# Optimization experiments

Hardware: AMD Instinct MI355X
Metric: run time of the kernel (lower is better)

## Reference

```python
import jax, jax.numpy as jnp
import numpy as np

H = 16          # num_heads
HD = 64         # head_dim = latent_dim // num_heads
RHD = 32        # rope_head_dim = head_dim // 2
NHD = 32        # nope_head_dim
Q_LAT = 256     # latent_dim // compression_ratio
KV_LAT = 204    # xf_latent_dim // (compression_ratio + 1)
MAX_LEN = 2048
THETA = 10000.0
EPS = 1e-5


def _rope_tables():
    half = RHD // 2  # 16
    freqs = 1.0 / THETA ** (np.arange(half, dtype=np.float32) / half)
    t = np.arange(MAX_LEN, dtype=np.float32)
    ang = np.outer(t, freqs)  # (MAX_LEN, half)
    return jnp.asarray(np.cos(ang)), jnp.asarray(np.sin(ang))

COS, SIN = _rope_tables()


def _ln(x, g, b):
    m = jnp.mean(x, axis=-1, keepdims=True)
    v = jnp.var(x, axis=-1, keepdims=True)
    return (x - m) * jax.lax.rsqrt(v + EPS) * g + b


def _rope(t, cos, sin):
    # t: (..., L, RHD); cos/sin: (L, RHD//2); interleaved even/odd convention
    ev, od = t[..., 0::2], t[..., 1::2]
    oe = ev * cos - od * sin
    oo = ev * sin + od * cos
    return jnp.stack([oe, oo], axis=-1).reshape(t.shape)


def setup_inputs() -> dict:
    key = jax.random.key(0)
    ks = jax.random.split(key, 12)
    D = 1024
    s = 0.02
    return {
        "x": jax.random.normal(ks[0], (2, 2048, D), jnp.float32),
        "xf": jax.random.normal(ks[1], (2, 2048, D), jnp.float32),
        "Wqc": jax.random.normal(ks[2], (D, Q_LAT), jnp.float32) * s,
        "gq": jnp.ones((Q_LAT,), jnp.float32),
        "bq": jnp.zeros((Q_LAT,), jnp.float32),
        "Wq_rope": jax.random.normal(ks[3], (Q_LAT, H * RHD), jnp.float32) * s,
        "Wq_nope": jax.random.normal(ks[4], (Q_LAT, H * NHD), jnp.float32) * s,
        "Wkvc": jax.random.normal(ks[5], (D, KV_LAT), jnp.float32) * s,
        "gkv": jnp.ones((KV_LAT,), jnp.float32),
        "bkv": jnp.zeros((KV_LAT,), jnp.float32),
        "Wk_nope": jax.random.normal(ks[6], (KV_LAT, H * NHD), jnp.float32) * s,
        "Wv": jax.random.normal(ks[7], (KV_LAT, H * HD), jnp.float32) * s,
        "Wkr": jax.random.normal(ks[8], (D, RHD), jnp.float32) * s,
        "Wo": jax.random.normal(ks[9], (D, D), jnp.float32) * s,
        "bo": jnp.zeros((D,), jnp.float32),
    }


def reference(x, xf, Wqc, gq, bq, Wq_rope, Wq_nope, Wkvc, gkv, bkv, Wk_nope, Wv, Wkr, Wo, bo):
    B, T, D = x.shape
    S = xf.shape[1]

    # query path: compress -> LN -> decoupled decompress
    ql = _ln(x @ Wqc, gq, bq)                                   # (B,T,Q_LAT)
    q_nope = (ql @ Wq_nope).reshape(B, T, H, NHD).transpose(0, 2, 1, 3)  # (B,H,T,NHD)
    q_rope = (ql @ Wq_rope).reshape(B, T, H, RHD).transpose(0, 2, 1, 3)  # (B,H,T,RHD)

    # key/value path: compress -> LN -> decompress; shared single rope head
    kvl = _ln(xf @ Wkvc, gkv, bkv)                              # (B,S,KV_LAT)
    k_nope = (kvl @ Wk_nope).reshape(B, S, H, NHD).transpose(0, 2, 1, 3)  # (B,H,S,NHD)
    v = (kvl @ Wv).reshape(B, S, H, HD).transpose(0, 2, 1, 3)   # (B,H,S,HD)
    k_rope = (xf @ Wkr).reshape(B, S, 1, RHD).transpose(0, 2, 1, 3)       # (B,1,S,RHD)

    q_rope = _rope(q_rope, COS[:T], SIN[:T])
    k_rope = _rope(k_rope, COS[:S], SIN[:S]) / H
    k_rope = jnp.broadcast_to(k_rope, (B, H, S, RHD))

    q = jnp.concatenate([q_nope, q_rope], axis=-1)              # (B,H,T,HD)
    k = jnp.concatenate([k_nope, k_rope], axis=-1)              # (B,H,S,HD)

    scale = 1.0 / jnp.sqrt(jnp.asarray(HD, q.dtype))
    scores = jnp.einsum("bhtd,bhsd->bhts", q, k) * scale
    attn = jax.nn.softmax(scores, axis=-1)
    o = jnp.einsum("bhts,bhsd->bhtd", attn, v)                  # (B,H,T,HD)
    o = o.transpose(0, 2, 1, 3).reshape(B, T, H * HD)
    return o @ Wo + bo
```

## Files before the change

### kernel.cpp

```cpp
#include <hip/hip_runtime.h>
#include <hip/hip_bf16.h>
#include <math.h>

#define SEQ 2048

typedef __bf16 bf16x8 __attribute__((ext_vector_type(8)));
typedef float  f32x4  __attribute__((ext_vector_type(4)));

__device__ __forceinline__ unsigned short f2bf(float f) {
  __bf16 h = (__bf16)f;
  return __builtin_bit_cast(unsigned short, h);
}

__device__ __forceinline__ void gload16(const unsigned short* g, unsigned short* l) {
  __builtin_amdgcn_global_load_lds(
      (const __attribute__((address_space(1))) void*)g,
      (__attribute__((address_space(3))) void*)l, 16, 0, 0);
}

#define CLOG (0.125f * 1.44269504f)

struct WPrep {
  const float* src[8];
  unsigned short* dst[8];
  int K[8], N[8], NR[8], KC[8], nb[8];
  float2* cst;
};

__global__ __launch_bounds__(256) void wprep_kernel(WPrep p)
{
  __shared__ float tile[32][33];
  int bid = blockIdx.x;
  if (bid < 128) {
    const int idx = bid * 256 + threadIdx.x;
    const int pos = idx >> 4, i = idx & 15;
    const float freq = exp2f(-(float)i * 0.8304820237f);
    const float ang = (float)pos * freq;
    p.cst[idx] = make_float2(cosf(ang), sinf(ang));
    return;
  }
  bid -= 128;
  int di = 0;
  while (bid >= p.nb[di]) { bid -= p.nb[di]; ++di; }
  const float* src = p.src[di];
  unsigned short* dst = p.dst[di];
  const int K = p.K[di], N = p.N[di], KC = p.KC[di];
  const int nkx = KC >> 5;
  const int k0 = (bid % nkx) * 32, n0 = (bid / nkx) * 32;
  const int tx = threadIdx.x & 31, ty = threadIdx.x >> 5;
  for (int r = ty; r < 32; r += 8) {
    const int k = k0 + r, n = n0 + tx;
    tile[r][tx] = (k < K && n < N) ? src[(long)k * N + n] : 0.0f;
  }
  __syncthreads();
  for (int r = ty; r < 32; r += 8) {
    const int n = n0 + r, k = k0 + tx;
    dst[(long)n * KC + k] = f2bf(tile[tx][r]);
  }
}

template <int EPI, bool AF32>
__device__ __forceinline__ void gemm_body(
    unsigned short* smem,
    const void* __restrict__ Av, const unsigned short* __restrict__ BT,
    const float* __restrict__ bias, const float2* __restrict__ cst,
    void* __restrict__ C0v, void* __restrict__ C1v, int K, int N,
    int bx, int by)
{
  unsigned short* As = smem;
  unsigned short* Bs = smem + 2 * 128 * 32;
  const int tid = threadIdx.x;
  const int w = tid >> 6, lane = tid & 63;
  const int ln16 = lane & 15, quad = lane >> 4;
  const int wm = (w >> 1) * 64, wn = (w & 1) * 64;
  const int m0 = by * 128, n0 = bx * 128;
  const int rr = tid >> 2, cc = (tid & 3) * 8;

  const unsigned short* A = (const unsigned short*)Av;
  const float* Af = (const float*)Av;

  auto stageB = [&](int ib, int k0) {
    gload16(&BT[(long)(n0 + rr)      * K + k0 + cc], &Bs[ib * 4096 + rr * 32 + cc]);
    gload16(&BT[(long)(n0 + 64 + rr) * K + k0 + cc], &Bs[ib * 4096 + (64 + rr) * 32 + cc]);
  };
  auto stageAbf = [&](int ib, int k0) {
    gload16(&A[(long)(m0 + rr)      * K + k0 + cc], &As[ib * 4096 + rr * 32 + cc]);
    gload16(&A[(long)(m0 + 64 + rr) * K + k0 + cc], &As[ib * 4096 + (64 + rr) * 32 + cc]);
  };
  auto writeAf32 = [&](int ib, const float4& a0, const float4& a1,
                       const float4& a2, const float4& a3) {
    ushort4 u;
    u.x = f2bf(a0.x); u.y = f2bf(a0.y); u.z = f2bf(a0.z); u.w = f2bf(a0.w);
    *(ushort4*)&As[ib * 4096 + rr * 32 + cc] = u;
    u.x = f2bf(a1.x); u.y = f2bf(a1.y); u.z = f2bf(a1.z); u.w = f2bf(a1.w);
    *(ushort4*)&As[ib * 4096 + rr * 32 + cc + 4] = u;
    u.x = f2bf(a2.x); u.y = f2bf(a2.y); u.z = f2bf(a2.z); u.w = f2bf(a2.w);
    *(ushort4*)&As[ib * 4096 + (64 + rr) * 32 + cc] = u;
    u.x = f2bf(a3.x); u.y = f2bf(a3.y); u.z = f2bf(a3.z); u.w = f2bf(a3.w);
    *(ushort4*)&As[ib * 4096 + (64 + rr) * 32 + cc + 4] = u;
  };

  f32x4 acc[4][4];
#pragma unroll
  for (int i = 0; i < 4; ++i)
#pragma unroll
    for (int j = 0; j < 4; ++j)
#pragma unroll
      for (int r = 0; r < 4; ++r) acc[i][j][r] = 0.0f;

  stageB(0, 0);
  if (AF32) {
    float4 a0 = *(const float4*)&Af[(long)(m0 + rr)      * K + cc];
    float4 a1 = *(const float4*)&Af[(long)(m0 + rr)      * K + cc + 4];
    float4 a2 = *(const float4*)&Af[(long)(m0 + 64 + rr) * K + cc];
    float4 a3 = *(const float4*)&Af[(long)(m0 + 64 + rr) * K + cc + 4];
    writeAf32(0, a0, a1, a2, a3);
  } else {
    stageAbf(0, 0);
  }

  int ib = 0;
  for (int k0 = 0; k0 < K; k0 += 32, ib ^= 1) {
    __syncthreads();
    const int kn = k0 + 32;
    float4 a0, a1, a2, a3;
    if (kn < K) {
      stageB(ib ^ 1, kn);
      if (AF32) {
        a0 = *(const float4*)&Af[(long)(m0 + rr)      * K + kn + cc];
        a1 = *(const float4*)&Af[(long)(m0 + rr)      * K + kn + cc + 4];
        a2 = *(const float4*)&Af[(long)(m0 + 64 + rr) * K + kn + cc];
        a3 = *(const float4*)&Af[(long)(m0 + 64 + rr) * K + kn + cc + 4];
      } else {
        stageAbf(ib ^ 1, kn);
      }
    }
    bf16x8 fa[4], fb[4];
#pragma unroll
    for (int i = 0; i < 4; ++i) fa[i] = *(const bf16x8*)&As[ib * 4096 + (wm + i * 16 + ln16) * 32 + quad * 8];
#pragma unroll
    for (int j = 0; j < 4; ++j) fb[j] = *(const bf16x8*)&Bs[ib * 4096 + (wn + j * 16 + ln16) * 32 + quad * 8];
#pragma unroll
    for (int i = 0; i < 4; ++i)
#pragma unroll
      for (int j = 0; j < 4; ++j)
        acc[i][j] = __builtin_amdgcn_mfma_f32_16x16x32_bf16(fa[i], fb[j], acc[i][j], 0, 0, 0);
    if (AF32 && kn < K) writeAf32(ib ^ 1, a0, a1, a2, a3);
  }

  if (EPI == 5 && n0 >= 512) {
    __syncthreads();
#pragma unroll
    for (int i = 0; i < 4; ++i) {
      const int rl = wm + i * 16 + quad * 4;
#pragma unroll
      for (int j = 0; j < 4; ++j) {
        const int cl = wn + j * 16 + ln16;
        ushort4 u;
        u.x = f2bf(acc[i][j][0]); u.y = f2bf(acc[i][j][1]);
        u.z = f2bf(acc[i][j][2]); u.w = f2bf(acc[i][j][3]);
        *(ushort4*)&smem[cl * 132 + rl] = u;
      }
    }
    __syncthreads();
    unsigned short* vT = (unsigned short*)C1v;
    const int b = m0 >> 11, sbase = m0 & (SEQ - 1);
    for (int q = tid; q < 128 * 16; q += 256) {
      const int cl = q >> 4, sch = (q & 15) * 8;
      bf16x8 val = *(const bf16x8*)&smem[cl * 132 + sch];
      const int c = (n0 - 512) + cl;
      const int hh = c >> 6, dd = c & 63;
      *(bf16x8*)&vT[((long)(b * 16 + hh) * 64 + dd) * SEQ + sbase + sch] = val;
    }
    return;
  }
#pragma unroll
  for (int i = 0; i < 4; ++i) {
    const int row0 = m0 + wm + i * 16 + quad * 4;
#pragma unroll
    for (int j = 0; j < 4; ++j) {
      const int col = n0 + wn + j * 16 + ln16;
      if (EPI == 0 || EPI == 1) {
        float* C = (float*)C0v;
        float bv = (EPI == 1) ? bias[col] : 0.0f;
#pragma unroll
        for (int r = 0; r < 4; ++r) C[(long)(row0 + r) * N + col] = acc[i][j][r] + bv;
      } else if (EPI == 3) {
        if (n0 < 512) {
          unsigned short* qn = (unsigned short*)C0v;
#pragma unroll
          for (int r = 0; r < 4; ++r) qn[(long)(row0 + r) * 512 + col] = f2bf(acc[i][j][r] * CLOG);
        } else {
          unsigned short* qr = (unsigned short*)C1v;
          const int c = col - 512;
          const int d = c & 31;
#pragma unroll
          for (int r = 0; r < 4; ++r) {
            const float v = acc[i][j][r];
            const float p = __shfl_xor(v, 1);
            const float2 t = cst[((row0 + r) & (SEQ - 1)) * 16 + (d >> 1)];
            const float o = ((d & 1) == 0) ? (v * t.x - p * t.y) : (p * t.y + v * t.x);
            qr[(long)(row0 + r) * 512 + c] = f2bf(o * CLOG);
          }
        }
      } else if (EPI == 4) {
        if (n0 < 256) {
          float* kvl = (float*)C0v;
#pragma unroll
          for (int r = 0; r < 4; ++r) kvl[(long)(row0 + r) * 256 + col] = acc[i][j][r];
        } else if (wn == 0 && j < 2) {
          unsigned short* kr = (unsigned short*)C1v;
          const int d = col - 256;
#pragma unroll
          for (int r = 0; r < 4; ++r) {
            const float v = acc[i][j][r];
            const float p = __shfl_xor(v, 1);
            const float2 t = cst[((row0 + r) & (SEQ - 1)) * 16 + (d >> 1)];
            const float o = ((d & 1) == 0) ? (v * t.x - p * t.y) : (p * t.y + v * t.x);
            kr[(long)(row0 + r) * 32 + d] = f2bf(o * 0.0625f);
          }
        }
      } else if (EPI == 5) {
        unsigned short* kn = (unsigned short*)C0v;
#pragma unroll
        for (int r = 0; r < 4; ++r) kn[(long)(row0 + r) * 512 + col] = f2bf(acc[i][j][r]);
      }
    }
  }
}

template <int EPI, bool AF32>
__global__ __launch_bounds__(256) void gemm_mfma(
    const void* __restrict__ Av, const unsigned short* __restrict__ BT,
    const float* __restrict__ bias, const float2* __restrict__ cst,
    void* __restrict__ C0v, void* __restrict__ C1v, int K, int N)
{
  __shared__ unsigned short smem[16896];
  gemm_body<EPI, AF32>(smem, Av, BT, bias, cst, C0v, C1v, K, N, blockIdx.x, blockIdx.y);
}

template <int E0, bool AF0, int E1, bool AF1>
__global__ __launch_bounds__(256) void gemm_dual(
    const void* __restrict__ A0, const unsigned short* __restrict__ BT0,
    void* __restrict__ C00, void* __restrict__ C01, int K0, int N0, int nx0,
    const void* __restrict__ A1, const unsigned short* __restrict__ BT1,
    void* __restrict__ C10, void* __restrict__ C11, int K1, int N1,
    const float2* __restrict__ cst)
{
  __shared__ unsigned short smem[16896];
  if (blockIdx.z == 0) {
    if ((int)blockIdx.x >= nx0) return;
    gemm_body<E0, AF0>(smem, A0, BT0, nullptr, cst, C00, C01, K0, N0, blockIdx.x, blockIdx.y);
  } else {
    gemm_body<E1, AF1>(smem, A1, BT1, nullptr, cst, C10, C11, K1, N1, blockIdx.x, blockIdx.y);
  }
}

__global__ __launch_bounds__(256) void ln2_kernel(
    const float* __restrict__ Xq, const float* __restrict__ Xkv,
    const float* __restrict__ gq, const float* __restrict__ bq,
    const float* __restrict__ gkv, const float* __restrict__ bkv,
    unsigned short* __restrict__ Yq, unsigned short* __restrict__ Ykv)
{
  const int row0 = blockIdx.x, tid = threadIdx.x;
  const bool isq = row0 < 4096;
  const int row = isq ? row0 : row0 - 4096;
  const float* X = isq ? Xq : Xkv;
  const float* g = isq ? gq : gkv;
  const float* b = isq ? bq : bkv;
  unsigned short* Y = isq ? Yq : Ykv;
  const int C = isq ? 256 : 204;
  const int Cp = isq ? 256 : 224;
  float v = (tid < C) ? X[(long)row * 256 + tid] : 0.0f;
  float s1 = v, s2 = v * v;
#pragma unroll
  for (int off = 1; off < 64; off <<= 1) {
    s1 += __shfl_xor(s1, off);
    s2 += __shfl_xor(s2, off);
  }
  __shared__ float rA[4], rB[4];
  const int wid = tid >> 6;
  if ((tid & 63) == 0) { rA[wid] = s1; rB[wid] = s2; }
  __syncthreads();
  s1 = rA[0] + rA[1] + rA[2] + rA[3];
  s2 = rB[0] + rB[1] + rB[2] + rB[3];
  const float mean = s1 / C;
  const float var  = s2 / C - mean * mean;
  const float r = rsqrtf(var + 1e-5f);
  if (tid < C) Y[(long)row * Cp + tid] = f2bf((v - mean) * r * g[tid] + b[tid]);
  else if (tid < Cp) Y[(long)row * Cp + tid] = 0;
}

#define KSTR 36
#define VSTR 68
#define PSTR 68
__global__ __launch_bounds__(256, 3) void attn_mfma_kernel(
    const unsigned short* __restrict__ qn, const unsigned short* __restrict__ qr,
    const unsigned short* __restrict__ kn, const unsigned short* __restrict__ kr,
    const unsigned short* __restrict__ vT, unsigned short* __restrict__ ob)
{
  __shared__ unsigned short Kn[2][64 * KSTR], Kr[2][64 * KSTR];
  __shared__ unsigned short Vs[2][64 * VSTR];
  __shared__ unsigned short Ps[64 * PSTR];
  const int id = blockIdx.x;
  const int xcd = id & 7, j = id >> 3;
  const int bh = xcd * 4 + (j & 3);
  const int tile = j >> 2;
  const int b = bh >> 4, h = bh & 15;
  const int t0 = tile * 64;
  const int tid = threadIdx.x;
  const int w = tid >> 6, lane = tid & 63;
  const int ln16 = lane & 15, quad = lane >> 4;
  const int trow = w * 16;
  const long bT = (long)b * SEQ;

  const int krow = tid >> 2, kc8 = (tid & 3) * 8;
  const int vd0 = tid >> 3, vc0 = (tid & 7) * 8;
  const int vd1 = vd0 + 32;

  bf16x8 q0 = *(const bf16x8*)&qn[(bT + t0 + trow + ln16) * 512 + h * 32 + quad * 8];
  bf16x8 q1 = *(const bf16x8*)&qr[(bT + t0 + trow + ln16) * 512 + h * 32 + quad * 8];

  auto loadKV = [&](int s0, bf16x8& rk0, bf16x8& rk1, bf16x8& rv0, bf16x8& rv1) {
    rk0 = *(const bf16x8*)&kn[(bT + s0 + krow) * 512 + h * 32 + kc8];
    rk1 = *(const bf16x8*)&kr[(bT + s0 + krow) * 32 + kc8];
    rv0 = *(const bf16x8*)&vT[((long)bh * 64 + vd0) * SEQ + s0 + vc0];
    rv1 = *(const bf16x8*)&vT[((long)bh * 64 + vd1) * SEQ + s0 + vc0];
  };
  auto writeKV = [&](int ib, bf16x8 rk0, bf16x8 rk1, bf16x8 rv0, bf16x8 rv1) {
    *(bf16x8*)&Kn[ib][krow * KSTR + kc8] = rk0;
    *(bf16x8*)&Kr[ib][krow * KSTR + kc8] = rk1;
    *(bf16x8*)&Vs[ib][vd0 * VSTR + vc0] = rv0;
    *(bf16x8*)&Vs[ib][vd1 * VSTR + vc0] = rv1;
  };

  bf16x8 ck0, ck1, cv0, cv1;
  bf16x8 nk0, nk1, nv0, nv1;
  loadKV(0, ck0, ck1, cv0, cv1);
  writeKV(0, ck0, ck1, cv0, cv1);
  loadKV(64, nk0, nk1, nv0, nv1);

  f32x4 o_acc[4];
#pragma unroll
  for (int nt = 0; nt < 4; ++nt)
#pragma unroll
    for (int r = 0; r < 4; ++r) o_acc[nt][r] = 0.0f;
  float l_i = 0.0f;

  int ib = 0;
  for (int s0 = 0; s0 < SEQ; s0 += 64, ib ^= 1) {
    __syncthreads();
    if (s0 + 64 < SEQ) {
      writeKV(ib ^ 1, nk0, nk1, nv0, nv1);
      if (s0 + 128 < SEQ) loadKV(s0 + 128, nk0, nk1, nv0, nv1);
    }

    f32x4 sf[4];
#pragma unroll
    for (int nt = 0; nt < 4; ++nt)
#pragma unroll
      for (int r = 0; r < 4; ++r) sf[nt][r] = 0.0f;
#pragma unroll
    for (int nt = 0; nt < 4; ++nt) {
      bf16x8 a0 = *(const bf16x8*)&Kn[ib][(nt * 16 + ln16) * KSTR + quad * 8];
      sf[nt] = __builtin_amdgcn_mfma_f32_16x16x32_bf16(a0, q0, sf[nt], 0, 0, 0);
      bf16x8 a1 = *(const bf16x8*)&Kr[ib][(nt * 16 + ln16) * KSTR + quad * 8];
      sf[nt] = __builtin_amdgcn_mfma_f32_16x16x32_bf16(a1, q1, sf[nt], 0, 0, 0);
    }

    float rs = 0.0f;
    float pv[4][4];
#pragma unroll
    for (int nt = 0; nt < 4; ++nt)
#pragma unroll
      for (int r = 0; r < 4; ++r) {
        const float p = exp2f(sf[nt][r]);
        pv[nt][r] = p;
        rs += p;
      }
    rs += __shfl_xor(rs, 16);
    rs += __shfl_xor(rs, 32);
    l_i += rs;
#pragma unroll
    for (int nt = 0; nt < 4; ++nt) {
      ushort4 u;
      u.x = f2bf(pv[nt][0]); u.y = f2bf(pv[nt][1]);
      u.z = f2bf(pv[nt][2]); u.w = f2bf(pv[nt][3]);
      *(ushort4*)&Ps[(trow + ln16) * PSTR + nt * 16 + quad * 4] = u;
    }

    bf16x8 a0 = *(const bf16x8*)&Ps[(trow + ln16) * PSTR + quad * 8];
    bf16x8 a1 = *(const bf16x8*)&Ps[(trow + ln16) * PSTR + 32 + quad * 8];
#pragma unroll
    for (int nt = 0; nt < 4; ++nt) {
      bf16x8 v0 = *(const bf16x8*)&Vs[ib][(nt * 16 + ln16) * VSTR + quad * 8];
      o_acc[nt] = __builtin_amdgcn_mfma_f32_16x16x32_bf16(a0, v0, o_acc[nt], 0, 0, 0);
      bf16x8 v1 = *(const bf16x8*)&Vs[ib][(nt * 16 + ln16) * VSTR + 32 + quad * 8];
      o_acc[nt] = __builtin_amdgcn_mfma_f32_16x16x32_bf16(a1, v1, o_acc[nt], 0, 0, 0);
    }
  }

  const float lr = 1.0f / l_i;
  float lq[4];
#pragma unroll
  for (int r = 0; r < 4; ++r) lq[r] = __shfl(lr, quad * 4 + r);
#pragma unroll
  for (int r = 0; r < 4; ++r) {
    const long t = t0 + trow + quad * 4 + r;
    const long base = (bT + t) * 1024 + h * 64 + ln16;
#pragma unroll
    for (int nt = 0; nt < 4; ++nt)
      ob[base + nt * 16] = f2bf(o_acc[nt][r] * lq[r]);
  }
}

extern "C" void kernel_launch(void* const* d_in, const int* in_sizes, int n_in,
                              void* d_out, int out_size, void* d_ws, size_t ws_size,
                              hipStream_t stream) {
  const float* x       = (const float*)d_in[0];
  const float* xf      = (const float*)d_in[1];
  const float* Wqc     = (const float*)d_in[2];
  const float* gq      = (const float*)d_in[3];
  const float* bq      = (const float*)d_in[4];
  const float* Wq_rope = (const float*)d_in[5];
  const float* Wq_nope = (const float*)d_in[6];
  const float* Wkvc    = (const float*)d_in[7];
  const float* gkv     = (const float*)d_in[8];
  const float* bkv     = (const float*)d_in[9];
  const float* Wk_nope = (const float*)d_in[10];
  const float* Wv      = (const float*)d_in[11];
  const float* Wkr     = (const float*)d_in[12];
  const float* Wo      = (const float*)d_in[13];
  const float* bo      = (const float*)d_in[14];
  float* out = (float*)d_out;

  const long R = 4096;
  float* ws = (float*)d_ws;
  float* ql_f  = ws;
  float* kvl_f = ql_f + R * 256;
  float2* cst  = (float2*)(kvl_f + R * 256);
  unsigned short* us = (unsigned short*)(cst + 2048 * 16);
  unsigned short* ql_bf  = us;  us += R * 256;
  unsigned short* kvl_bf = us;  us += R * 224;
  unsigned short* qn_bf  = us;  us += R * 512;
  unsigned short* qr_bf  = us;  us += R * 512;
  unsigned short* kn_bf  = us;  us += R * 512;
  unsigned short* kr_bf  = us;  us += R * 32;
  unsigned short* vT_bf  = us;  us += R * 1024;
  unsigned short* o_bf   = us;  us += R * 1024;
  unsigned short* WqcT   = us;  us += 256 * 1024;
  unsigned short* WkvkrT = us;  us += 384 * 1024;
  unsigned short* WqnqrT = us;  us += 1024 * 256;
  unsigned short* WknvT  = us;  us += 1536 * 224;
  unsigned short* WoT    = us;  us += 1024 * 1024;

  WPrep p;
  const float* srcs[8] = {Wqc, Wkvc, Wkr, Wq_nope, Wq_rope, Wk_nope, Wv, Wo};
  unsigned short* dsts[8] = {WqcT, WkvkrT, WkvkrT + 256 * 1024,
                             WqnqrT, WqnqrT + 512 * 256,
                             WknvT, WknvT + 512 * 224, WoT};
  const int Ks[8]  = {1024, 1024, 1024, 256, 256, 204, 204, 1024};
  const int Ns[8]  = {256, 204, 32, 512, 512, 512, 1024, 1024};
  const int NRs[8] = {256, 256, 128, 512, 512, 512, 1024, 1024};
  const int KCs[8] = {1024, 1024, 1024, 256, 256, 224, 224, 1024};
  int total = 128;
  for (int i = 0; i < 8; ++i) {
    p.src[i] = srcs[i]; p.dst[i] = dsts[i];
    p.K[i] = Ks[i]; p.N[i] = Ns[i]; p.NR[i] = NRs[i]; p.KC[i] = KCs[i];
    p.nb[i] = (KCs[i] / 32) * (NRs[i] / 32);
    total += p.nb[i];
  }
  p.cst = cst;
  wprep_kernel<<<total, 256, 0, stream>>>(p);

  gemm_dual<0, true, 4, true><<<dim3(3, 32, 2), 256, 0, stream>>>(
      x, WqcT, ql_f, nullptr, 1024, 256, 2,
      xf, WkvkrT, kvl_f, kr_bf, 1024, 384, cst);
  ln2_kernel<<<8192, 256, 0, stream>>>(ql_f, kvl_f, gq, bq, gkv, bkv, ql_bf, kvl_bf);
  gemm_dual<3, false, 5, false><<<dim3(12, 32, 2), 256, 0, stream>>>(
      ql_bf, WqnqrT, qn_bf, qr_bf, 256, 1024, 8,
      kvl_bf, WknvT, kn_bf, vT_bf, 224, 1536, cst);
  attn_mfma_kernel<<<1024, 256, 0, stream>>>(qn_bf, qr_bf, kn_bf, kr_bf, vT_bf, o_bf);
  gemm_mfma<1, false><<<dim3(8, 32), 256, 0, stream>>>(o_bf, WoT, bo, nullptr, out, nullptr, 1024, 1024);
}
```

Measured before the change: 260.3 us.

## Use 64x64 GEMM tiles for compress and output projections; keep K-rope in registers

```diff
diff --git a/kernel.cpp b/kernel.cpp
--- a/kernel.cpp
+++ b/kernel.cpp
@@ -77,7 +77,6 @@
   const int rr = tid >> 2, cc = (tid & 3) * 8;
 
   const unsigned short* A = (const unsigned short*)Av;
-  const float* Af = (const float*)Av;
 
   auto stageB = [&](int ib, int k0) {
     gload16(&BT[(long)(n0 + rr)      * K + k0 + cc], &Bs[ib * 4096 + rr * 32 + cc]);
@@ -87,18 +86,6 @@
     gload16(&A[(long)(m0 + rr)      * K + k0 + cc], &As[ib * 4096 + rr * 32 + cc]);
     gload16(&A[(long)(m0 + 64 + rr) * K + k0 + cc], &As[ib * 4096 + (64 + rr) * 32 + cc]);
   };
-  auto writeAf32 = [&](int ib, const float4& a0, const float4& a1,
-                       const float4& a2, const float4& a3) {
-    ushort4 u;
-    u.x = f2bf(a0.x); u.y = f2bf(a0.y); u.z = f2bf(a0.z); u.w = f2bf(a0.w);
-    *(ushort4*)&As[ib * 4096 + rr * 32 + cc] = u;
-    u.x = f2bf(a1.x); u.y = f2bf(a1.y); u.z = f2bf(a1.z); u.w = f2bf(a1.w);
-    *(ushort4*)&As[ib * 4096 + rr * 32 + cc + 4] = u;
-    u.x = f2bf(a2.x); u.y = f2bf(a2.y); u.z = f2bf(a2.z); u.w = f2bf(a2.w);
-    *(ushort4*)&As[ib * 4096 + (64 + rr) * 32 + cc] = u;
-    u.x = f2bf(a3.x); u.y = f2bf(a3.y); u.z = f2bf(a3.z); u.w = f2bf(a3.w);
-    *(ushort4*)&As[ib * 4096 + (64 + rr) * 32 + cc + 4] = u;
-  };
 
   f32x4 acc[4][4];
 #pragma unroll
@@ -109,32 +96,13 @@
       for (int r = 0; r < 4; ++r) acc[i][j][r] = 0.0f;
 
   stageB(0, 0);
-  if (AF32) {
-    float4 a0 = *(const float4*)&Af[(long)(m0 + rr)      * K + cc];
-    float4 a1 = *(const float4*)&Af[(long)(m0 + rr)      * K + cc + 4];
-    float4 a2 = *(const float4*)&Af[(long)(m0 + 64 + rr) * K + cc];
-    float4 a3 = *(const float4*)&Af[(long)(m0 + 64 + rr) * K + cc + 4];
-    writeAf32(0, a0, a1, a2, a3);
-  } else {
-    stageAbf(0, 0);
-  }
+  stageAbf(0, 0);
 
   int ib = 0;
   for (int k0 = 0; k0 < K; k0 += 32, ib ^= 1) {
     __syncthreads();
     const int kn = k0 + 32;
-    float4 a0, a1, a2, a3;
-    if (kn < K) {
-      stageB(ib ^ 1, kn);
-      if (AF32) {
-        a0 = *(const float4*)&Af[(long)(m0 + rr)      * K + kn + cc];
-        a1 = *(const float4*)&Af[(long)(m0 + rr)      * K + kn + cc + 4];
-        a2 = *(const float4*)&Af[(long)(m0 + 64 + rr) * K + kn + cc];
-        a3 = *(const float4*)&Af[(long)(m0 + 64 + rr) * K + kn + cc + 4];
-      } else {
-        stageAbf(ib ^ 1, kn);
-      }
-    }
+    if (kn < K) { stageB(ib ^ 1, kn); stageAbf(ib ^ 1, kn); }
     bf16x8 fa[4], fb[4];
 #pragma unroll
     for (int i = 0; i < 4; ++i) fa[i] = *(const bf16x8*)&As[ib * 4096 + (wm + i * 16 + ln16) * 32 + quad * 8];
@@ -145,7 +113,6 @@
 #pragma unroll
       for (int j = 0; j < 4; ++j)
         acc[i][j] = __builtin_amdgcn_mfma_f32_16x16x32_bf16(fa[i], fb[j], acc[i][j], 0, 0, 0);
-    if (AF32 && kn < K) writeAf32(ib ^ 1, a0, a1, a2, a3);
   }
 
   if (EPI == 5 && n0 >= 512) {
@@ -180,12 +147,7 @@
 #pragma unroll
     for (int j = 0; j < 4; ++j) {
       const int col = n0 + wn + j * 16 + ln16;
-      if (EPI == 0 || EPI == 1) {
-        float* C = (float*)C0v;
-        float bv = (EPI == 1) ? bias[col] : 0.0f;
-#pragma unroll
-        for (int r = 0; r < 4; ++r) C[(long)(row0 + r) * N + col] = acc[i][j][r] + bv;
-      } else if (EPI == 3) {
+      if (EPI == 3) {
         if (n0 < 512) {
           unsigned short* qn = (unsigned short*)C0v;
 #pragma unroll
@@ -203,12 +165,127 @@
             qr[(long)(row0 + r) * 512 + c] = f2bf(o * CLOG);
           }
         }
+      } else if (EPI == 5) {
+        unsigned short* kn = (unsigned short*)C0v;
+#pragma unroll
+        for (int r = 0; r < 4; ++r) kn[(long)(row0 + r) * 512 + col] = f2bf(acc[i][j][r]);
+      }
+    }
+  }
+}
+
+template <int E0, bool AF0, int E1, bool AF1>
+__global__ __launch_bounds__(256) void gemm_dual(
+    const void* __restrict__ A0, const unsigned short* __restrict__ BT0,
+    void* __restrict__ C00, void* __restrict__ C01, int K0, int N0, int nx0,
+    const void* __restrict__ A1, const unsigned short* __restrict__ BT1,
+    void* __restrict__ C10, void* __restrict__ C11, int K1, int N1,
+    const float2* __restrict__ cst)
+{
+  __shared__ unsigned short smem[16896];
+  if (blockIdx.z == 0) {
+    if ((int)blockIdx.x >= nx0) return;
+    gemm_body<E0, AF0>(smem, A0, BT0, nullptr, cst, C00, C01, K0, N0, blockIdx.x, blockIdx.y);
+  } else {
+    gemm_body<E1, AF1>(smem, A1, BT1, nullptr, cst, C10, C11, K1, N1, blockIdx.x, blockIdx.y);
+  }
+}
+
+template <int EPI, bool AF32>
+__device__ __forceinline__ void gemm_body64(
+    unsigned short* smem,
+    const void* __restrict__ Av, const unsigned short* __restrict__ BT,
+    const float* __restrict__ bias, const float2* __restrict__ cst,
+    void* __restrict__ C0v, void* __restrict__ C1v, int K, int N,
+    int bx, int by)
+{
+  unsigned short* As = smem;
+  unsigned short* Bs = smem + 2 * 64 * 32;
+  const int tid = threadIdx.x;
+  const int w = tid >> 6, lane = tid & 63;
+  const int ln16 = lane & 15, quad = lane >> 4;
+  const int wm = (w >> 1) * 32, wn = (w & 1) * 32;
+  const int m0 = by * 64, n0 = bx * 64;
+  const int rr = tid >> 2, cc = (tid & 3) * 8;
+
+  const unsigned short* A = (const unsigned short*)Av;
+  const float* Af = (const float*)Av;
+
+  auto stageB = [&](int ib, int k0) {
+    gload16(&BT[(long)(n0 + rr) * K + k0 + cc], &Bs[ib * 2048 + rr * 32 + cc]);
+  };
+  auto stageAbf = [&](int ib, int k0) {
+    gload16(&A[(long)(m0 + rr) * K + k0 + cc], &As[ib * 2048 + rr * 32 + cc]);
+  };
+  auto writeAf32 = [&](int ib, const float4& a0, const float4& a1) {
+    ushort4 u;
+    u.x = f2bf(a0.x); u.y = f2bf(a0.y); u.z = f2bf(a0.z); u.w = f2bf(a0.w);
+    *(ushort4*)&As[ib * 2048 + rr * 32 + cc] = u;
+    u.x = f2bf(a1.x); u.y = f2bf(a1.y); u.z = f2bf(a1.z); u.w = f2bf(a1.w);
+    *(ushort4*)&As[ib * 2048 + rr * 32 + cc + 4] = u;
+  };
+
+  f32x4 acc[2][2];
+#pragma unroll
+  for (int i = 0; i < 2; ++i)
+#pragma unroll
+    for (int j = 0; j < 2; ++j)
+#pragma unroll
+      for (int r = 0; r < 4; ++r) acc[i][j][r] = 0.0f;
+
+  stageB(0, 0);
+  if (AF32) {
+    float4 a0 = *(const float4*)&Af[(long)(m0 + rr) * K + cc];
+    float4 a1 = *(const float4*)&Af[(long)(m0 + rr) * K + cc + 4];
+    writeAf32(0, a0, a1);
+  } else {
+    stageAbf(0, 0);
+  }
+
+  int ib = 0;
+  for (int k0 = 0; k0 < K; k0 += 32, ib ^= 1) {
+    __syncthreads();
+    const int kn = k0 + 32;
+    float4 a0, a1;
+    if (kn < K) {
+      stageB(ib ^ 1, kn);
+      if (AF32) {
+        a0 = *(const float4*)&Af[(long)(m0 + rr) * K + kn + cc];
+        a1 = *(const float4*)&Af[(long)(m0 + rr) * K + kn + cc + 4];
+      } else {
+        stageAbf(ib ^ 1, kn);
+      }
+    }
+    bf16x8 fa[2], fb[2];
+#pragma unroll
+    for (int i = 0; i < 2; ++i) fa[i] = *(const bf16x8*)&As[ib * 2048 + (wm + i * 16 + ln16) * 32 + quad * 8];
+#pragma unroll
+    for (int j = 0; j < 2; ++j) fb[j] = *(const bf16x8*)&Bs[ib * 2048 + (wn + j * 16 + ln16) * 32 + quad * 8];
+#pragma unroll
+    for (int i = 0; i < 2; ++i)
+#pragma unroll
+      for (int j = 0; j < 2; ++j)
+        acc[i][j] = __builtin_amdgcn_mfma_f32_16x16x32_bf16(fa[i], fb[j], acc[i][j], 0, 0, 0);
+    if (AF32 && kn < K) writeAf32(ib ^ 1, a0, a1);
+  }
+
+#pragma unroll
+  for (int i = 0; i < 2; ++i) {
+    const int row0 = m0 + wm + i * 16 + quad * 4;
+#pragma unroll
+    for (int j = 0; j < 2; ++j) {
+      const int col = n0 + wn + j * 16 + ln16;
+      if (EPI == 0 || EPI == 1) {
+        float* C = (float*)C0v;
+        float bv = (EPI == 1) ? bias[col] : 0.0f;
+#pragma unroll
+        for (int r = 0; r < 4; ++r) C[(long)(row0 + r) * N + col] = acc[i][j][r] + bv;
       } else if (EPI == 4) {
         if (n0 < 256) {
           float* kvl = (float*)C0v;
 #pragma unroll
           for (int r = 0; r < 4; ++r) kvl[(long)(row0 + r) * 256 + col] = acc[i][j][r];
-        } else if (wn == 0 && j < 2) {
+        } else if (wn == 0) {
           unsigned short* kr = (unsigned short*)C1v;
           const int d = col - 256;
 #pragma unroll
@@ -220,39 +297,35 @@
             kr[(long)(row0 + r) * 32 + d] = f2bf(o * 0.0625f);
           }
         }
-      } else if (EPI == 5) {
-        unsigned short* kn = (unsigned short*)C0v;
-#pragma unroll
-        for (int r = 0; r < 4; ++r) kn[(long)(row0 + r) * 512 + col] = f2bf(acc[i][j][r]);
       }
     }
   }
 }
 
 template <int EPI, bool AF32>
-__global__ __launch_bounds__(256) void gemm_mfma(
+__global__ __launch_bounds__(256) void gemm_mfma64(
     const void* __restrict__ Av, const unsigned short* __restrict__ BT,
     const float* __restrict__ bias, const float2* __restrict__ cst,
     void* __restrict__ C0v, void* __restrict__ C1v, int K, int N)
 {
-  __shared__ unsigned short smem[16896];
-  gemm_body<EPI, AF32>(smem, Av, BT, bias, cst, C0v, C1v, K, N, blockIdx.x, blockIdx.y);
+  __shared__ unsigned short smem[8192];
+  gemm_body64<EPI, AF32>(smem, Av, BT, bias, cst, C0v, C1v, K, N, blockIdx.x, blockIdx.y);
 }
 
 template <int E0, bool AF0, int E1, bool AF1>
-__global__ __launch_bounds__(256) void gemm_dual(
+__global__ __launch_bounds__(256) void gemm_dual64(
     const void* __restrict__ A0, const unsigned short* __restrict__ BT0,
     void* __restrict__ C00, void* __restrict__ C01, int K0, int N0, int nx0,
     const void* __restrict__ A1, const unsigned short* __restrict__ BT1,
     void* __restrict__ C10, void* __restrict__ C11, int K1, int N1,
     const float2* __restrict__ cst)
 {
-  __shared__ unsigned short smem[16896];
+  __shared__ unsigned short smem[8192];
   if (blockIdx.z == 0) {
     if ((int)blockIdx.x >= nx0) return;
-    gemm_body<E0, AF0>(smem, A0, BT0, nullptr, cst, C00, C01, K0, N0, blockIdx.x, blockIdx.y);
+    gemm_body64<E0, AF0>(smem, A0, BT0, nullptr, cst, C00, C01, K0, N0, blockIdx.x, blockIdx.y);
   } else {
-    gemm_body<E1, AF1>(smem, A1, BT1, nullptr, cst, C10, C11, K1, N1, blockIdx.x, blockIdx.y);
+    gemm_body64<E1, AF1>(smem, A1, BT1, nullptr, cst, C10, C11, K1, N1, blockIdx.x, blockIdx.y);
   }
 }
 
@@ -294,12 +367,12 @@
 #define KSTR 36
 #define VSTR 68
 #define PSTR 68
-__global__ __launch_bounds__(256, 3) void attn_mfma_kernel(
+__global__ __launch_bounds__(256, 4) void attn_mfma_kernel(
     const unsigned short* __restrict__ qn, const unsigned short* __restrict__ qr,
     const unsigned short* __restrict__ kn, const unsigned short* __restrict__ kr,
     const unsigned short* __restrict__ vT, unsigned short* __restrict__ ob)
 {
-  __shared__ unsigned short Kn[2][64 * KSTR], Kr[2][64 * KSTR];
+  __shared__ unsigned short Kn[2][64 * KSTR];
   __shared__ unsigned short Vs[2][64 * VSTR];
   __shared__ unsigned short Ps[64 * PSTR];
   const int id = blockIdx.x;
@@ -321,24 +394,30 @@
   bf16x8 q0 = *(const bf16x8*)&qn[(bT + t0 + trow + ln16) * 512 + h * 32 + quad * 8];
   bf16x8 q1 = *(const bf16x8*)&qr[(bT + t0 + trow + ln16) * 512 + h * 32 + quad * 8];
 
-  auto loadKV = [&](int s0, bf16x8& rk0, bf16x8& rk1, bf16x8& rv0, bf16x8& rv1) {
+  auto loadKV = [&](int s0, bf16x8& rk0, bf16x8& rv0, bf16x8& rv1) {
     rk0 = *(const bf16x8*)&kn[(bT + s0 + krow) * 512 + h * 32 + kc8];
-    rk1 = *(const bf16x8*)&kr[(bT + s0 + krow) * 32 + kc8];
     rv0 = *(const bf16x8*)&vT[((long)bh * 64 + vd0) * SEQ + s0 + vc0];
     rv1 = *(const bf16x8*)&vT[((long)bh * 64 + vd1) * SEQ + s0 + vc0];
   };
-  auto writeKV = [&](int ib, bf16x8 rk0, bf16x8 rk1, bf16x8 rv0, bf16x8 rv1) {
+  auto writeKV = [&](int ib, bf16x8 rk0, bf16x8 rv0, bf16x8 rv1) {
     *(bf16x8*)&Kn[ib][krow * KSTR + kc8] = rk0;
-    *(bf16x8*)&Kr[ib][krow * KSTR + kc8] = rk1;
     *(bf16x8*)&Vs[ib][vd0 * VSTR + vc0] = rv0;
     *(bf16x8*)&Vs[ib][vd1 * VSTR + vc0] = rv1;
   };
-
-  bf16x8 ck0, ck1, cv0, cv1;
-  bf16x8 nk0, nk1, nv0, nv1;
-  loadKV(0, ck0, ck1, cv0, cv1);
-  writeKV(0, ck0, ck1, cv0, cv1);
-  loadKV(64, nk0, nk1, nv0, nv1);
+  auto loadKrF = [&](int s0, bf16x8* f) {
+#pragma unroll
+    for (int nt = 0; nt < 4; ++nt)
+      f[nt] = *(const bf16x8*)&kr[(bT + s0 + nt * 16 + ln16) * 32 + quad * 8];
+  };
+
+  bf16x8 ck0, cv0, cv1;
+  bf16x8 nk0, nv0, nv1;
+  bf16x8 ckr[4], nkr[4];
+  loadKV(0, ck0, cv0, cv1);
+  writeKV(0, ck0, cv0, cv1);
+  loadKV(64, nk0, nv0, nv1);
+  loadKrF(0, ckr);
+  loadKrF(64, nkr);
 
   f32x4 o_acc[4];
 #pragma unroll
@@ -351,8 +430,8 @@
   for (int s0 = 0; s0 < SEQ; s0 += 64, ib ^= 1) {
     __syncthreads();
     if (s0 + 64 < SEQ) {
-      writeKV(ib ^ 1, nk0, nk1, nv0, nv1);
-      if (s0 + 128 < SEQ) loadKV(s0 + 128, nk0, nk1, nv0, nv1);
+      writeKV(ib ^ 1, nk0, nv0, nv1);
+      if (s0 + 128 < SEQ) loadKV(s0 + 128, nk0, nv0, nv1);
     }
 
     f32x4 sf[4];
@@ -364,9 +443,12 @@
     for (int nt = 0; nt < 4; ++nt) {
       bf16x8 a0 = *(const bf16x8*)&Kn[ib][(nt * 16 + ln16) * KSTR + quad * 8];
       sf[nt] = __builtin_amdgcn_mfma_f32_16x16x32_bf16(a0, q0, sf[nt], 0, 0, 0);
-      bf16x8 a1 = *(const bf16x8*)&Kr[ib][(nt * 16 + ln16) * KSTR + quad * 8];
-      sf[nt] = __builtin_amdgcn_mfma_f32_16x16x32_bf16(a1, q1, sf[nt], 0, 0, 0);
-    }
+      sf[nt] = __builtin_amdgcn_mfma_f32_16x16x32_bf16(ckr[nt], q1, sf[nt], 0, 0, 0);
+    }
+
+#pragma unroll
+    for (int nt = 0; nt < 4; ++nt) ckr[nt] = nkr[nt];
+    if (s0 + 128 < SEQ) loadKrF(s0 + 128, nkr);
 
     float rs = 0.0f;
     float pv[4][4];
@@ -473,13 +555,13 @@
   p.cst = cst;
   wprep_kernel<<<total, 256, 0, stream>>>(p);
 
-  gemm_dual<0, true, 4, true><<<dim3(3, 32, 2), 256, 0, stream>>>(
-      x, WqcT, ql_f, nullptr, 1024, 256, 2,
+  gemm_dual64<0, true, 4, true><<<dim3(6, 64, 2), 256, 0, stream>>>(
+      x, WqcT, ql_f, nullptr, 1024, 256, 4,
       xf, WkvkrT, kvl_f, kr_bf, 1024, 384, cst);
   ln2_kernel<<<8192, 256, 0, stream>>>(ql_f, kvl_f, gq, bq, gkv, bkv, ql_bf, kvl_bf);
   gemm_dual<3, false, 5, false><<<dim3(12, 32, 2), 256, 0, stream>>>(
       ql_bf, WqnqrT, qn_bf, qr_bf, 256, 1024, 8,
       kvl_bf, WknvT, kn_bf, vT_bf, 224, 1536, cst);
   attn_mfma_kernel<<<1024, 256, 0, stream>>>(qn_bf, qr_bf, kn_bf, kr_bf, vT_bf, o_bf);
-  gemm_mfma<1, false><<<dim3(8, 32), 256, 0, stream>>>(o_bf, WoT, bo, nullptr, out, nullptr, 1024, 1024);
-}
+  gemm_mfma64<1, false><<<dim3(16, 64), 256, 0, stream>>>(o_bf, WoT, bo, nullptr, out, nullptr, 1024, 1024);
+}
```

After: 246.6 us. -5.3%, faster.
